# Kernel optimization log

Measured on AMD Instinct MI355X. Metric: run time of the kernel, lower is better.

## Reference

```python
import jax, jax.numpy as jnp
import numpy as np

# Paired binary-tree layout over 20 inputs: widths 20->10->5->3->2->1.
# Odd trailing element is carried through unchanged. Node counts per layer
# sum to 19 nodes per tree; 19 trees total.
LAYER_WIDTHS = [20, 10, 5, 3, 2]  # widths at the input of each pairing layer
NODE_COUNTS = [10, 5, 2, 1, 1]    # pairs formed at each layer (sum = 19)
EPS = 1e-6


def setup_inputs() -> dict:
    key = jax.random.key(0)
    k1, k2, k3, k4 = jax.random.split(key, 4)
    B = 1_000_000
    p1 = jax.random.randint(k1, (B,), 0, 10)
    p2 = jax.random.randint(k2, (B,), 0, 10)
    c20 = jax.random.uniform(k3, (B, 20), dtype=jnp.float32)  # fuzzy truth values in [0,1]
    # raw andness params: one per node (19) per tree (19)
    w_raw = jax.random.normal(k4, (19, 19), dtype=jnp.float32)
    return {"p1": p1, "p2": p2, "c20": c20, "w_raw": w_raw}


def _multi_tree_forward(c20, w_raw):
    B = c20.shape[0]
    T = 19  # number of trees
    # andness in (0,1): convex mix between AND (min) and OR (max)
    w = jax.nn.sigmoid(w_raw)  # [T, 19]
    # all 19 trees see the same 20D input -> vectorize trees as a dim
    x = jnp.broadcast_to(c20[:, None, :], (B, T, 20))  # [B, T, 20]
    off = 0
    for width, n in zip(LAYER_WIDTHS, NODE_COUNTS):
        a = x[:, :, 0:2 * n:2]   # left children  [B, T, n]
        b = x[:, :, 1:2 * n:2]   # right children [B, T, n]
        wn = w[:, off:off + n][None, :, :]  # [1, T, n]
        y = wn * jnp.minimum(a, b) + (1.0 - wn) * jnp.maximum(a, b)
        if width % 2 == 1:  # carry the unpaired trailing element through
            y = jnp.concatenate([y, x[:, :, -1:]], axis=-1)
        x = y
        off += n
    out = x[:, :, 0]  # [B, 19] root of each tree
    return jnp.clip(out, EPS, 1.0 - EPS)


def reference(p1, p2, c20, w_raw):
    # p1/p2 are part of the original signature but unused by the forward math
    return _multi_tree_forward(c20, w_raw)
```

## Files before the change

kernel.cpp:

```cpp
#include <hip/hip_runtime.h>

#define EPS_F 1e-6f
#define BLK   256
#define SPB   256

__global__ void sigmoid_w_kernel(const float* __restrict__ w_raw,
                                 float* __restrict__ w) {
    int i = threadIdx.x;
    if (i < 361) {
        w[i] = 1.0f / (1.0f + expf(-w_raw[i]));
    }
}

__device__ __forceinline__ float mixf(float a, float b, float wv) {
    float mn = fminf(a, b);
    float mx = fmaxf(a, b);
    return fmaf(wv, mn - mx, mx);
}

__global__ __launch_bounds__(BLK) void tree_forward_kernel(
    const float* __restrict__ c20,
    const float* __restrict__ w,
    float* __restrict__ out,
    int B)
{
    __shared__ float so[SPB * 19];

    const int tid = threadIdx.x;
    const long long S0 = (long long)blockIdx.x * SPB;
    const long long s  = S0 + tid;

    float x[20];
    if (s < B) {
        const float4* p = reinterpret_cast<const float4*>(c20 + s * 20);
        #pragma unroll
        for (int q = 0; q < 5; ++q) {
            float4 v = p[q];
            x[4*q+0] = v.x; x[4*q+1] = v.y; x[4*q+2] = v.z; x[4*q+3] = v.w;
        }
    } else {
        #pragma unroll
        for (int i = 0; i < 20; ++i) x[i] = 0.0f;
    }

    float* __restrict__ o = &so[tid * 19];

    #pragma unroll
    for (int t = 0; t < 19; ++t) {
        const float* wr = w + t * 19;

        float y[10];
        #pragma unroll
        for (int k = 0; k < 10; ++k)
            y[k] = mixf(x[2*k], x[2*k+1], wr[k]);

        float z[5];
        #pragma unroll
        for (int k = 0; k < 5; ++k)
            z[k] = mixf(y[2*k], y[2*k+1], wr[10 + k]);

        float u0 = mixf(z[0], z[1], wr[15]);
        float u1 = mixf(z[2], z[3], wr[16]);
        float u2 = z[4];

        float v0 = mixf(u0, u1, wr[17]);

        float r = mixf(v0, u2, wr[18]);

        o[t] = fminf(fmaxf(r, EPS_F), 1.0f - EPS_F);
    }

    __syncthreads();

    const long long nDw    = (long long)B * 19;
    const long long baseDw = S0 * 19;
    const float4* ls = reinterpret_cast<const float4*>(so);

    #pragma unroll
    for (int i = tid; i < (SPB * 19) / 4; i += BLK) {
        long long g = baseDw + (long long)i * 4;
        if (g + 3 < nDw) {
            *reinterpret_cast<float4*>(out + g) = ls[i];
        } else if (g < nDw) {
            float4 v = ls[i];
            out[g] = v.x;
            if (g + 1 < nDw) out[g + 1] = v.y;
            if (g + 2 < nDw) out[g + 2] = v.z;
        }
    }
}

extern "C" void kernel_launch(void* const* d_in, const int* in_sizes, int n_in,
                              void* d_out, int out_size, void* d_ws, size_t ws_size,
                              hipStream_t stream) {
    const float* c20   = (const float*)d_in[2];
    const float* w_raw = (const float*)d_in[3];
    float* out = (float*)d_out;
    float* w   = (float*)d_ws;

    int B = in_sizes[0];

    sigmoid_w_kernel<<<1, 384, 0, stream>>>(w_raw, w);

    int grid = (B + SPB - 1) / SPB;
    tree_forward_kernel<<<grid, BLK, 0, stream>>>(c20, w, out, B);
}
```

Before: 155.7 us.

## Use persistent per-wave slabs with wave-local barriers and hoist first-layer min/max

Replaces one-block-per-256-samples with a capped grid of persistent blocks. Each wavefront processes 64-sample slabs in a grid-stride loop and stores results through its own shared-memory slab, synchronised by a wave barrier instead of a block-wide __syncthreads. The first-layer min/max and difference are computed once per sample instead of once per tree. Occupancy is hinted through launch bounds. Together these aim to cut block-level synchronisation and redundant ALU work, at the cost of relying on wave-level LDS ordering and a fixed grid cap.

```diff
diff --git a/kernel.cpp b/kernel.cpp
--- a/kernel.cpp
+++ b/kernel.cpp
@@ -2,7 +2,8 @@
 
 #define EPS_F 1e-6f
 #define BLK   256
-#define SPB   256
+#define WPB   4
+#define GRID  2048
 
 __global__ void sigmoid_w_kernel(const float* __restrict__ w_raw,
                                  float* __restrict__ w) {
@@ -18,74 +19,88 @@
     return fmaf(wv, mn - mx, mx);
 }
 
-__global__ __launch_bounds__(BLK) void tree_forward_kernel(
+__global__ __launch_bounds__(BLK, 8) void tree_forward_kernel(
     const float* __restrict__ c20,
     const float* __restrict__ w,
     float* __restrict__ out,
     int B)
 {
-    __shared__ float so[SPB * 19];
+    __shared__ float so[WPB][64 * 19];
 
-    const int tid = threadIdx.x;
-    const long long S0 = (long long)blockIdx.x * SPB;
-    const long long s  = S0 + tid;
+    const int lane = threadIdx.x & 63;
+    const int wid  = threadIdx.x >> 6;
+    float* __restrict__ slab = so[wid];
 
-    float x[20];
-    if (s < B) {
-        const float4* p = reinterpret_cast<const float4*>(c20 + s * 20);
+    const long long nSlab  = ((long long)B + 63) >> 6;
+    const long long stride = (long long)gridDim.x * WPB;
+
+    for (long long sl = (long long)blockIdx.x * WPB + wid; sl < nSlab; sl += stride) {
+        const long long s = sl * 64 + lane;
+
+        float x[20];
+        if (s < B) {
+            const float4* p = reinterpret_cast<const float4*>(c20 + s * 20);
+            #pragma unroll
+            for (int q = 0; q < 5; ++q) {
+                float4 v = p[q];
+                x[4*q+0] = v.x; x[4*q+1] = v.y; x[4*q+2] = v.z; x[4*q+3] = v.w;
+            }
+        } else {
+            #pragma unroll
+            for (int i = 0; i < 20; ++i) x[i] = 0.0f;
+        }
+
+        float mx[10], d[10];
         #pragma unroll
-        for (int q = 0; q < 5; ++q) {
-            float4 v = p[q];
-            x[4*q+0] = v.x; x[4*q+1] = v.y; x[4*q+2] = v.z; x[4*q+3] = v.w;
+        for (int k = 0; k < 10; ++k) {
+            float a = x[2*k], b = x[2*k+1];
+            float mn = fminf(a, b);
+            mx[k] = fmaxf(a, b);
+            d[k]  = mn - mx[k];
         }
-    } else {
+
         #pragma unroll
-        for (int i = 0; i < 20; ++i) x[i] = 0.0f;
-    }
+        for (int t = 0; t < 19; ++t) {
+            const float* wr = w + t * 19;
 
-    float* __restrict__ o = &so[tid * 19];
+            float y[10];
+            #pragma unroll
+            for (int k = 0; k < 10; ++k)
+                y[k] = fmaf(wr[k], d[k], mx[k]);
 
-    #pragma unroll
-    for (int t = 0; t < 19; ++t) {
-        const float* wr = w + t * 19;
+            float z[5];
+            #pragma unroll
+            for (int k = 0; k < 5; ++k)
+                z[k] = mixf(y[2*k], y[2*k+1], wr[10 + k]);
 
-        float y[10];
-        #pragma unroll
-        for (int k = 0; k < 10; ++k)
-            y[k] = mixf(x[2*k], x[2*k+1], wr[k]);
+            float u0 = mixf(z[0], z[1], wr[15]);
+            float u1 = mixf(z[2], z[3], wr[16]);
 
-        float z[5];
-        #pragma unroll
-        for (int k = 0; k < 5; ++k)
-            z[k] = mixf(y[2*k], y[2*k+1], wr[10 + k]);
+            float v0 = mixf(u0, u1, wr[17]);
 
-        float u0 = mixf(z[0], z[1], wr[15]);
-        float u1 = mixf(z[2], z[3], wr[16]);
-        float u2 = z[4];
+            float r = mixf(v0, z[4], wr[18]);
 
-        float v0 = mixf(u0, u1, wr[17]);
+            slab[lane * 19 + t] = fminf(fmaxf(r, EPS_F), 1.0f - EPS_F);
+        }
 
-        float r = mixf(v0, u2, wr[18]);
+        __builtin_amdgcn_s_waitcnt(0xC07F);
+        __builtin_amdgcn_wave_barrier();
 
-        o[t] = fminf(fmaxf(r, EPS_F), 1.0f - EPS_F);
-    }
-
-    __syncthreads();
-
-    const long long nDw    = (long long)B * 19;
-    const long long baseDw = S0 * 19;
-    const float4* ls = reinterpret_cast<const float4*>(so);
-
-    #pragma unroll
-    for (int i = tid; i < (SPB * 19) / 4; i += BLK) {
-        long long g = baseDw + (long long)i * 4;
-        if (g + 3 < nDw) {
-            *reinterpret_cast<float4*>(out + g) = ls[i];
-        } else if (g < nDw) {
-            float4 v = ls[i];
-            out[g] = v.x;
-            if (g + 1 < nDw) out[g + 1] = v.y;
-            if (g + 2 < nDw) out[g + 2] = v.z;
+        const long long slabBase = sl * 1216;
+        if (sl * 64 + 64 <= (long long)B) {
+            const float4* ls = reinterpret_cast<const float4*>(slab);
+            float4* gd = reinterpret_cast<float4*>(out + slabBase);
+            #pragma unroll
+            for (int i = 0; i < 5; ++i) {
+                int idx = lane + i * 64;
+                if (idx < 304) gd[idx] = ls[idx];
+            }
+        } else {
+            const long long nDw = (long long)B * 19;
+            for (int i = lane; i < 1216; i += 64) {
+                long long g = slabBase + i;
+                if (g < nDw) out[g] = slab[i];
+            }
         }
     }
 }
@@ -102,6 +117,8 @@
 
     sigmoid_w_kernel<<<1, 384, 0, stream>>>(w_raw, w);
 
-    int grid = (B + SPB - 1) / SPB;
+    long long nSlab = ((long long)B + 63) >> 6;
+    int grid = (int)((nSlab + WPB - 1) / WPB);
+    if (grid > GRID) grid = GRID;
     tree_forward_kernel<<<grid, BLK, 0, stream>>>(c20, w, out, B);
 }
```

New measurement: 161.7 us. 1.04x slower.
